# Kernel tuning notes

Measured on AMD Instinct MI355X. Metric: run time of the kernel, lower is better.

Reference implementation:

```python
import jax, jax.numpy as jnp
import numpy as np
from jax import lax

S = 512  # number of sampled points (module init arg s)
BIG = 1e10  # stand-in for +inf, safe in low precision


def _fps_indices(xyz, s):
    """Farthest point sampling. xyz: [B,N,3] -> idx [B,s] int32.
    Deterministic start at point 0 (torch impl uses a random start; math is identical
    apart from the seed point)."""
    B, N, _ = xyz.shape

    def step(carry, _):
        dists, last_idx = carry  # dists [B,N], last_idx [B]
        centroid = jnp.take_along_axis(xyz, last_idx[:, None, None], axis=1)  # [B,1,3]
        d = jnp.sum((xyz - centroid) ** 2, axis=-1)  # [B,N] squared L2
        dists = jnp.minimum(dists, d)
        nxt = jnp.argmax(dists, axis=-1).astype(jnp.int32)  # farthest from current set
        return (dists, nxt), last_idx

    init = (jnp.full((B, N), BIG, xyz.dtype), jnp.zeros((B,), jnp.int32))
    _, idxs = lax.scan(step, init, None, length=s)  # idxs [s,B]
    return jnp.transpose(idxs)  # [B,s]


def _index_points(points, idx):
    # points [B,N,C], idx [B,s] -> [B,s,C]
    return jnp.take_along_axis(points, idx[:, :, None], axis=1)


def setup_inputs() -> dict:
    key = jax.random.key(0)
    k1, k2 = jax.random.split(key)
    xyz = jax.random.normal(k1, (16, 65536, 3), dtype=jnp.float32)
    f = jax.random.normal(k2, (16, 65536, 64), dtype=jnp.float32)
    return {"xyz": xyz, "f": f}


def reference(xyz, f):
    idx = _fps_indices(xyz, S)              # [B,S]
    xyz_sampled = _index_points(xyz, idx)   # [B,S,3]
    f_sampled = _index_points(f, idx)       # [B,S,C]
    return (xyz_sampled, f_sampled)
```

## Files before the change

### kernel.cpp

```cpp
#include <hip/hip_runtime.h>


#define NB   16
#define NPTS 65536
#define NS   512
#define WPB  16
#define CHUNK (NPTS / WPB)
#define NTHR 256
#define PPT  (CHUNK / NTHR)
#define NWAVE (NTHR / 64)
#define SPW  (NS / WPB)

__device__ __forceinline__ float sqdist3(float x, float y, float z,
                                         float cx, float cy, float cz) {
    float dx = __fsub_rn(x, cx);
    float dy = __fsub_rn(y, cy);
    float dz = __fsub_rn(z, cz);
    return __fadd_rn(__fadd_rn(__fmul_rn(dx, dx), __fmul_rn(dy, dy)),
                     __fmul_rn(dz, dz));
}

__global__ void __launch_bounds__(NTHR, 1)
fps_kernel(const float* __restrict__ xyz, const float* __restrict__ feat,
           float* __restrict__ out, unsigned long long* __restrict__ slots) {
    const int wg   = blockIdx.x & (WPB - 1);
    const int b    = blockIdx.x / WPB;
    const int tid  = threadIdx.x;
    const int lane = tid & 63;
    const int wave = tid >> 6;

    __shared__ int   sel[NS];
    __shared__ float cent[3];
    __shared__ float wbd[NWAVE];
    __shared__ int   wbi[NWAVE];

    const float* bx  = xyz + (size_t)b * NPTS * 3;
    const int   base = wg * CHUNK;

    float rx[PPT], ry[PPT], rz[PPT], dmin[PPT];
#pragma unroll
    for (int k = 0; k < PPT; ++k) {
        int g = base + tid + k * NTHR;
        rx[k] = bx[3 * g + 0];
        ry[k] = bx[3 * g + 1];
        rz[k] = bx[3 * g + 2];
        dmin[k] = 1e10f;
    }

    if (tid == 0) {
        sel[0] = 0;
        cent[0] = bx[0]; cent[1] = bx[1]; cent[2] = bx[2];
    }
    __syncthreads();

    for (int it = 1; it < NS; ++it) {
        const float cx = cent[0], cy = cent[1], cz = cent[2];
        float bd = -1.0f; int bi = 0;
#pragma unroll
        for (int k = 0; k < PPT; ++k) {
            float d  = sqdist3(rx[k], ry[k], rz[k], cx, cy, cz);
            float dm = fminf(dmin[k], d);
            dmin[k] = dm;
            if (dm > bd) { bd = dm; bi = base + tid + k * NTHR; }
        }
        for (int off = 32; off >= 1; off >>= 1) {
            float od = __shfl_down(bd, off, 64);
            int   oi = __shfl_down(bi, off, 64);
            if (od > bd || (od == bd && oi < bi)) { bd = od; bi = oi; }
        }
        if (lane == 0) { wbd[wave] = bd; wbi[wave] = bi; }
        __syncthreads();
        if (tid == 0) {
            for (int w = 1; w < NWAVE; ++w) {
                float od = wbd[w]; int oi = wbi[w];
                if (od > bd || (od == bd && oi < bi)) { bd = od; bi = oi; }
            }
            unsigned long long v =
                ((unsigned long long)__float_as_uint(bd) << 32) |
                ((unsigned long long)(unsigned)it << 16) |
                (unsigned long long)(unsigned)bi;
            __hip_atomic_store(
                &slots[((size_t)(it & 1) * NB + b) * WPB + wg], v,
                __ATOMIC_RELAXED, __HIP_MEMORY_SCOPE_AGENT);
        }
        if (wave == 0 && lane < WPB) {
            unsigned long long* sp =
                &slots[((size_t)(it & 1) * NB + b) * WPB + lane];
            unsigned long long v;
            for (;;) {
                v = __hip_atomic_load(sp, __ATOMIC_RELAXED,
                                      __HIP_MEMORY_SCOPE_AGENT);
                if (((unsigned)(v >> 16) & 0xFFFFu) == (unsigned)it) break;
                __builtin_amdgcn_s_sleep(1);
            }
            float d2 = __uint_as_float((unsigned)(v >> 32));
            int   i2 = (int)(v & 0xFFFFu);
            float px = bx[3 * i2 + 0];
            float py = bx[3 * i2 + 1];
            float pz = bx[3 * i2 + 2];
            int   wl = lane;
            for (int off = 8; off >= 1; off >>= 1) {
                float od = __shfl_down(d2, off, 64);
                int   oi = __shfl_down(i2, off, 64);
                int   ol = __shfl_down(wl, off, 64);
                if (lane + off < WPB) {
                    if (od > d2 || (od == d2 && oi < i2)) {
                        d2 = od; i2 = oi; wl = ol;
                    }
                }
            }
            int w = __shfl(wl, 0, 64);
            float wxc = __shfl(px, w, 64);
            float wyc = __shfl(py, w, 64);
            float wzc = __shfl(pz, w, 64);
            if (lane == 0) {
                sel[it] = i2;
                cent[0] = wxc; cent[1] = wyc; cent[2] = wzc;
            }
        }
        __syncthreads();
    }

    const float* bf   = feat + (size_t)b * NPTS * 64;
    float*       oxyz = out + (size_t)b * NS * 3;
    float*       of   = out + (size_t)NB * NS * 3 + (size_t)b * NS * 64;
    const int c  = tid & 63;
    const int sr = tid >> 6;
    for (int k = 0; k < SPW / NWAVE; ++k) {
        int s = wg * SPW + k * NWAVE + sr;
        int p = sel[s];
        of[(size_t)s * 64 + c] = bf[(size_t)p * 64 + c];
    }
    if (tid < SPW * 3) {
        int s    = wg * SPW + tid / 3;
        int comp = tid % 3;
        oxyz[s * 3 + comp] = bx[sel[s] * 3 + comp];
    }
}

extern "C" void kernel_launch(void* const* d_in, const int* in_sizes, int n_in,
                              void* d_out, int out_size, void* d_ws, size_t ws_size,
                              hipStream_t stream) {
    const float* xyz = (const float*)d_in[0];
    const float* f   = (const float*)d_in[1];
    float* out = (float*)d_out;
    unsigned long long* slots = (unsigned long long*)d_ws;
    hipMemsetAsync(d_ws, 0, (size_t)2 * NB * WPB * sizeof(unsigned long long),
                   stream);
    fps_kernel<<<dim3(NB * WPB), dim3(NTHR), 0, stream>>>(xyz, f, out, slots);
}
```

Baseline: 1.531 ms.

## Pack max/index into 64-bit keys and broadcast centroid coords through slots

Distance and index are packed into one 64-bit key, so the wave reduction becomes a single xor-shuffle max. Each workgroup's winning thread publishes its key plus the winner's x/y/z coordinates to global slots with tagged atomic exchanges. Every wave then polls all slots itself and computes the centroid locally. This removes one of the two block barriers per iteration, the dependent global load of the winning point's coordinates, and the serial tid-0 merge. The cost is four atomics per workgroup per iteration and every wave spinning on global memory, with no sleep in the poll loop.

```diff
diff --git a/kernel.cpp b/kernel.cpp
--- a/kernel.cpp
+++ b/kernel.cpp
@@ -8,8 +8,9 @@
 #define CHUNK (NPTS / WPB)
 #define NTHR 256
 #define PPT  (CHUNK / NTHR)
-#define NWAVE (NTHR / 64)
+#define NWAVE 4
 #define SPW  (NS / WPB)
+#define SLOTW (4 * WPB)
 
 __device__ __forceinline__ float sqdist3(float x, float y, float z,
                                          float cx, float cy, float cz) {
@@ -29,10 +30,8 @@
     const int lane = tid & 63;
     const int wave = tid >> 6;
 
-    __shared__ int   sel[NS];
-    __shared__ float cent[3];
-    __shared__ float wbd[NWAVE];
-    __shared__ int   wbi[NWAVE];
+    __shared__ int sel[NS];
+    __shared__ unsigned long long wmax[NWAVE];
 
     const float* bx  = xyz + (size_t)b * NPTS * 3;
     const int   base = wg * CHUNK;
@@ -47,14 +46,10 @@
         dmin[k] = 1e10f;
     }
 
-    if (tid == 0) {
-        sel[0] = 0;
-        cent[0] = bx[0]; cent[1] = bx[1]; cent[2] = bx[2];
-    }
-    __syncthreads();
+    float cx = bx[0], cy = bx[1], cz = bx[2];
+    if (tid == 0) sel[0] = 0;
 
     for (int it = 1; it < NS; ++it) {
-        const float cx = cent[0], cy = cent[1], cz = cent[2];
         float bd = -1.0f; int bi = 0;
 #pragma unroll
         for (int k = 0; k < PPT; ++k) {
@@ -63,63 +58,66 @@
             dmin[k] = dm;
             if (dm > bd) { bd = dm; bi = base + tid + k * NTHR; }
         }
-        for (int off = 32; off >= 1; off >>= 1) {
-            float od = __shfl_down(bd, off, 64);
-            int   oi = __shfl_down(bi, off, 64);
-            if (od > bd || (od == bd && oi < bi)) { bd = od; bi = oi; }
+        unsigned long long packed =
+            ((unsigned long long)__float_as_uint(bd) << 16) |
+            (unsigned long long)(0xFFFF - bi);
+        unsigned long long wv = packed;
+        for (int off = 1; off < 64; off <<= 1) {
+            unsigned long long o = __shfl_xor(wv, off, 64);
+            if (o > wv) wv = o;
         }
-        if (lane == 0) { wbd[wave] = bd; wbi[wave] = bi; }
+        if (lane == 0) wmax[wave] = wv;
         __syncthreads();
-        if (tid == 0) {
-            for (int w = 1; w < NWAVE; ++w) {
-                float od = wbd[w]; int oi = wbi[w];
-                if (od > bd || (od == bd && oi < bi)) { bd = od; bi = oi; }
-            }
-            unsigned long long v =
-                ((unsigned long long)__float_as_uint(bd) << 32) |
-                ((unsigned long long)(unsigned)it << 16) |
-                (unsigned long long)(unsigned)bi;
-            __hip_atomic_store(
-                &slots[((size_t)(it & 1) * NB + b) * WPB + wg], v,
-                __ATOMIC_RELAXED, __HIP_MEMORY_SCOPE_AGENT);
+        unsigned long long m0 = wmax[0], m1 = wmax[1];
+        unsigned long long m2 = wmax[2], m3 = wmax[3];
+        if (m1 > m0) m0 = m1;
+        if (m3 > m2) m2 = m3;
+        if (m2 > m0) m0 = m2;
+
+        unsigned long long* sb =
+            slots + ((size_t)(it & 1) * NB + b) * SLOTW;
+
+        if (packed == m0) {
+            int g = 0xFFFF - (int)(m0 & 0xFFFFull);
+            int k = (g - base - tid) >> 8;
+            float wx = rx[0], wy = ry[0], wz = rz[0];
+#pragma unroll
+            for (int j = 1; j < PPT; ++j)
+                if (j == k) { wx = rx[j]; wy = ry[j]; wz = rz[j]; }
+            unsigned long long tag = (unsigned long long)it << 48;
+            __hip_atomic_exchange(&sb[0 * WPB + wg], tag | m0,
+                                  __ATOMIC_RELAXED, __HIP_MEMORY_SCOPE_AGENT);
+            __hip_atomic_exchange(&sb[1 * WPB + wg],
+                                  tag | (unsigned long long)__float_as_uint(wx),
+                                  __ATOMIC_RELAXED, __HIP_MEMORY_SCOPE_AGENT);
+            __hip_atomic_exchange(&sb[2 * WPB + wg],
+                                  tag | (unsigned long long)__float_as_uint(wy),
+                                  __ATOMIC_RELAXED, __HIP_MEMORY_SCOPE_AGENT);
+            __hip_atomic_exchange(&sb[3 * WPB + wg],
+                                  tag | (unsigned long long)__float_as_uint(wz),
+                                  __ATOMIC_RELAXED, __HIP_MEMORY_SCOPE_AGENT);
         }
-        if (wave == 0 && lane < WPB) {
-            unsigned long long* sp =
-                &slots[((size_t)(it & 1) * NB + b) * WPB + lane];
-            unsigned long long v;
-            for (;;) {
-                v = __hip_atomic_load(sp, __ATOMIC_RELAXED,
-                                      __HIP_MEMORY_SCOPE_AGENT);
-                if (((unsigned)(v >> 16) & 0xFFFFu) == (unsigned)it) break;
-                __builtin_amdgcn_s_sleep(1);
-            }
-            float d2 = __uint_as_float((unsigned)(v >> 32));
-            int   i2 = (int)(v & 0xFFFFu);
-            float px = bx[3 * i2 + 0];
-            float py = bx[3 * i2 + 1];
-            float pz = bx[3 * i2 + 2];
-            int   wl = lane;
-            for (int off = 8; off >= 1; off >>= 1) {
-                float od = __shfl_down(d2, off, 64);
-                int   oi = __shfl_down(i2, off, 64);
-                int   ol = __shfl_down(wl, off, 64);
-                if (lane + off < WPB) {
-                    if (od > d2 || (od == d2 && oi < i2)) {
-                        d2 = od; i2 = oi; wl = ol;
-                    }
-                }
-            }
-            int w = __shfl(wl, 0, 64);
-            float wxc = __shfl(px, w, 64);
-            float wyc = __shfl(py, w, 64);
-            float wzc = __shfl(pz, w, 64);
-            if (lane == 0) {
-                sel[it] = i2;
-                cent[0] = wxc; cent[1] = wyc; cent[2] = wzc;
-            }
+
+        unsigned long long v;
+        for (;;) {
+            v = __hip_atomic_load(&sb[lane], __ATOMIC_RELAXED,
+                                  __HIP_MEMORY_SCOPE_AGENT);
+            if ((v >> 48) == (unsigned long long)it) break;
         }
-        __syncthreads();
+        int sidx = lane & 15;
+        unsigned long long cand = __shfl(v, sidx, 64);
+        int ws = sidx;
+        for (int off = 1; off < 16; off <<= 1) {
+            unsigned long long oc = __shfl_xor(cand, off, 64);
+            int               os = __shfl_xor(ws, off, 64);
+            if (oc > cand) { cand = oc; ws = os; }
+        }
+        cx = __uint_as_float((unsigned)__shfl(v, 16 + ws, 64));
+        cy = __uint_as_float((unsigned)__shfl(v, 32 + ws, 64));
+        cz = __uint_as_float((unsigned)__shfl(v, 48 + ws, 64));
+        if (tid == 0) sel[it] = 0xFFFF - (int)(cand & 0xFFFFull);
     }
+    __syncthreads();
 
     const float* bf   = feat + (size_t)b * NPTS * 64;
     float*       oxyz = out + (size_t)b * NS * 3;
@@ -145,7 +143,7 @@
     const float* f   = (const float*)d_in[1];
     float* out = (float*)d_out;
     unsigned long long* slots = (unsigned long long*)d_ws;
-    hipMemsetAsync(d_ws, 0, (size_t)2 * NB * WPB * sizeof(unsigned long long),
+    hipMemsetAsync(d_ws, 0, (size_t)2 * NB * SLOTW * sizeof(unsigned long long),
                    stream);
     fps_kernel<<<dim3(NB * WPB), dim3(NTHR), 0, stream>>>(xyz, f, out, slots);
 }
```

Result: slower. 1.795 ms (+17.2%).
